# Kernel tuning notes

Measured on AMD Instinct MI355X. Metric: run time of the kernel, lower is better.

## Reference

```python
import jax, jax.numpy as jnp
import numpy as np

WIDTH = 384  # reconstruction grid is WIDTH x WIDTH


def _conv2d(x, w, b, pad):
    y = jax.lax.conv_general_dilated(
        x, w, window_strides=(1, 1), padding=[(pad, pad), (pad, pad)],
        dimension_numbers=('NCHW', 'OIHW', 'NCHW'))
    return y + b[None, :, None, None]


def _backproject(sino, angles, width):
    """Pixel-driven flat-detector fan-beam backprojection with linear interp.
    torch-radon FanBeam defaults: src_dist = det_dist = det_count,
    det_spacing = (src_dist + det_dist) / src_dist.
    sino: [B, C, A, D] -> image [B, C, width, width]."""
    B, C, A, D = sino.shape
    dsrc = float(D)
    ddet = float(D)
    spacing = (dsrc + ddet) / dsrc  # = 2.0
    c = jnp.arange(width, dtype=sino.dtype) - (width - 1) / 2.0
    X = c[None, None, :]   # [1,1,W] image x
    Y = c[None, :, None]   # [1,W,1] image y
    cb = jnp.cos(angles)[:, None, None]  # [A,1,1]
    sb = jnp.sin(angles)[:, None, None]
    px = cb * X + sb * Y    # pixel coords in rotated (source) frame, [A,W,W]
    py = -sb * X + cb * Y
    # fractional detector coordinate of the ray source->pixel
    s = px * ((dsrc + ddet) / spacing) / (dsrc + py) + (D - 1) / 2.0
    i0 = jnp.floor(s)
    frac = s - i0
    i0 = i0.astype(jnp.int32)
    i1 = i0 + 1
    WW = width * width
    w0 = jnp.where((i0 >= 0) & (i0 < D), 1.0 - frac, 0.0).reshape(A, WW)
    w1 = jnp.where((i1 >= 0) & (i1 < D), frac, 0.0).reshape(A, WW)
    i0c = jnp.clip(i0, 0, D - 1).reshape(A, WW)
    i1c = jnp.clip(i1, 0, D - 1).reshape(A, WW)

    def gather(idx):
        return jnp.take_along_axis(
            sino, jnp.broadcast_to(idx[None, None], (B, C, A, WW)), axis=3)

    out = (gather(i0c) * w0 + gather(i1c) * w1).sum(axis=2)  # sum over angles
    return out.reshape(B, C, width, width)


def setup_inputs() -> dict:
    key = jax.random.key(0)
    ks = jax.random.split(key, 5)
    A, D = 192, 576
    sino = jax.random.normal(ks[0], (1, 1, A, D), dtype=jnp.float32)
    angles = (jnp.arange(A, dtype=jnp.float32) * (2.0 * np.pi / A))
    w1 = jax.random.normal(ks[1], (16, 1, 5, 5), dtype=jnp.float32) * 0.05
    b1 = jnp.zeros((16,), dtype=jnp.float32)
    w2 = jax.random.normal(ks[2], (1, 16, 5, 5), dtype=jnp.float32) * 0.05
    b2 = jnp.zeros((1,), dtype=jnp.float32)
    w3 = jax.random.normal(ks[3], (1, 2, 3, 3), dtype=jnp.float32) * 0.05
    b3 = jnp.zeros((1,), dtype=jnp.float32)
    return {"sino": sino, "angles": angles, "w1": w1, "b1": b1,
            "w2": w2, "b2": b2, "w3": w3, "b3": b3}


def reference(sino, angles, w1, b1, w2, b2, w3, b3):
    img = _backproject(sino, angles, WIDTH)
    h = _conv2d(sino, w1, b1, pad=2)
    sino_pred = _conv2d(h, w2, b2, pad=2)
    img_sino = _backproject(sino_pred, angles, WIDTH)
    img_pred = _conv2d(jnp.concatenate([img, img_sino], axis=1), w3, b3, pad=1)
    return (sino_pred, img_sino, img_pred)
```

## Files before the change

### kernel.cpp

```cpp
#include <hip/hip_runtime.h>

#define A_N 192
#define D_N 576
#define W_N 384
#define NPIX (W_N * W_N)
#define NSIN (A_N * D_N)
#define RSTR 580

__global__ __launch_bounds__(256, 1) void conv9_kernel(
    const float* __restrict__ sino, const float* __restrict__ angles,
    const float* __restrict__ w1, const float* __restrict__ b1,
    const float* __restrict__ w2, const float* __restrict__ b2,
    float* __restrict__ sino_pred, float2* __restrict__ inter,
    float4* __restrict__ tab)
{
    __shared__ float t[16][40];
    __shared__ float sw1[400], sw2[400], sb1[16];
    __shared__ float K[625], wsb1[25];
    __shared__ float Wcs[9][81];
    __shared__ float biasc[9];

    int tid = threadIdx.x;
    int byi = blockIdx.x / 18;
    int bxi = blockIdx.x % 18;
    int y0 = byi * 8, x0 = bxi * 32;

    if (blockIdx.x == 0) {
        if (tid < A_N) {
            float s, c;
            sincosf(angles[tid], &s, &c);
            tab[tid] = make_float4(c, s, fmaf(576.f, c, -287.5f * s),
                                         fmaf(576.f, s,  287.5f * c));
        }
        for (int i = tid; i < A_N * 4; i += 256) {
            int a = i >> 2, j = i & 3;
            inter[a * RSTR + (j < 2 ? j : 576 + j)] = make_float2(0.f, 0.f);
        }
    }

    for (int i = tid; i < 640; i += 256) {
        int r = i / 40, c = i - r * 40;
        int gy = y0 - 4 + r, gx = x0 - 4 + c;
        t[r][c] = (gy >= 0 && gy < A_N && gx >= 0 && gx < D_N)
                ? sino[gy * D_N + gx] : 0.f;
    }
    for (int i = tid; i < 400; i += 256) { sw1[i] = w1[i]; sw2[i] = w2[i]; }
    if (tid < 16) sb1[tid] = b1[tid];
    __syncthreads();

    for (int i = tid; i < 625; i += 256) {
        int q = i / 25, r = i - q * 25;
        float acc = 0.f;
        #pragma unroll
        for (int c = 0; c < 16; ++c)
            acc = fmaf(sw2[c * 25 + q], sw1[c * 25 + r], acc);
        K[i] = acc;
    }
    if (tid < 25) {
        float acc = 0.f;
        #pragma unroll
        for (int c = 0; c < 16; ++c) acc = fmaf(sw2[c * 25 + tid], sb1[c], acc);
        wsb1[tid] = acc;
    }
    __syncthreads();

    int ylo = (y0 == 0) ? 0 : 2, yhi = (y0 == A_N - 8) ? 4 : 2;
    int xlo = (x0 == 0) ? 0 : 2, xhi = (x0 == D_N - 32) ? 4 : 2;
    int nx = xhi - xlo + 1;
    int nc = (yhi - ylo + 1) * nx;

    for (int e = tid; e < nc * 81; e += 256) {
        int ci = e / 81, s = e - ci * 81;
        int yc = ylo + ci / nx, xc = xlo + ci % nx;
        int sy = s / 9 - 4, sx = s % 9 - 4;
        float acc = 0.f;
        for (int qy = -2; qy <= 2; ++qy) {
            if ((yc == 0 && qy < 0) || (yc == 1 && qy < -1) ||
                (yc == 3 && qy > 1) || (yc == 4 && qy > 0)) continue;
            int vy = sy - qy; if (vy < -2 || vy > 2) continue;
            for (int qx = -2; qx <= 2; ++qx) {
                if ((xc == 0 && qx < 0) || (xc == 1 && qx < -1) ||
                    (xc == 3 && qx > 1) || (xc == 4 && qx > 0)) continue;
                int vx = sx - qx; if (vx < -2 || vx > 2) continue;
                acc += K[((qy + 2) * 5 + qx + 2) * 25 + (vy + 2) * 5 + (vx + 2)];
            }
        }
        Wcs[ci][s] = acc;
    }
    if (tid < nc) {
        int yc = ylo + tid / nx, xc = xlo + tid % nx;
        float acc = b2[0];
        for (int qy = -2; qy <= 2; ++qy) {
            if ((yc == 0 && qy < 0) || (yc == 1 && qy < -1) ||
                (yc == 3 && qy > 1) || (yc == 4 && qy > 0)) continue;
            for (int qx = -2; qx <= 2; ++qx) {
                if ((xc == 0 && qx < 0) || (xc == 1 && qx < -1) ||
                    (xc == 3 && qx > 1) || (xc == 4 && qx > 0)) continue;
                acc += wsb1[(qy + 2) * 5 + qx + 2];
            }
        }
        biasc[tid] = acc;
    }
    __syncthreads();

    int lr = tid >> 5, lc = tid & 31;
    int gy = y0 + lr, gx = x0 + lc;
    int yc = (gy <= 1) ? gy : ((gy >= A_N - 2) ? (gy - (A_N - 5)) : 2);
    int xc = (gx <= 1) ? gx : ((gx >= D_N - 2) ? (gx - (D_N - 5)) : 2);
    int ci = (yc - ylo) * nx + (xc - xlo);
    float acc = biasc[ci];
    const float* Wp = Wcs[ci];
    #pragma unroll
    for (int sy = 0; sy < 9; ++sy)
        #pragma unroll
        for (int sx = 0; sx < 9; ++sx)
            acc = fmaf(t[lr + sy][lc + sx], Wp[sy * 9 + sx], acc);
    sino_pred[gy * D_N + gx] = acc;
    inter[gy * RSTR + 2 + gx] = make_float2(t[lr + 4][lc + 4], acc);
}

__global__ __launch_bounds__(256) void backproject2_kernel(
    const float2* __restrict__ inter, const float4* __restrict__ tab,
    float2* __restrict__ part2)
{
    int tid = threadIdx.x;
    int seg = blockIdx.z;
    int a0 = seg * 64;
    int tx = tid & 15, ty = tid >> 4;
    int gx = blockIdx.x * 16 + tx;
    int gy = blockIdx.y * 16 + ty;
    int idx = gy * W_N + gx;
    float X = (float)gx - 191.5f;
    float Y = (float)gy - 191.5f;
    float acc0 = 0.f, acc1 = 0.f;
    const float2* base = inter + (size_t)a0 * RSTR + 2;
    #pragma unroll 8
    for (int i = 0; i < 64; ++i) {
        float4 tb = tab[a0 + i];
        float den = fmaf(tb.x, Y, fmaf(-tb.y, X, 576.f));
        float num = fmaf(tb.z, X, fmaf(tb.w, Y, 165600.f));
        float s   = num * __builtin_amdgcn_rcpf(den);
        float sc  = fminf(fmaxf(s, -2.f), 576.f);
        float fl  = floorf(sc);
        float fr  = sc - fl;
        int   ic  = (int)fl;
        float4 v = *reinterpret_cast<const float4*>(base + (size_t)i * RSTR + ic);
        acc0 = fmaf(v.x, 1.f - fr, fmaf(v.z, fr, acc0));
        acc1 = fmaf(v.y, 1.f - fr, fmaf(v.w, fr, acc1));
    }
    part2[seg * NPIX + idx] = make_float2(acc0, acc1);
}

__global__ __launch_bounds__(256) void conv3_kernel(
    const float2* __restrict__ part2,
    const float* __restrict__ w3, const float* __restrict__ b3,
    float* __restrict__ img_sino, float* __restrict__ img_pred)
{
    __shared__ float t0[10][34], t1[10][34];
    __shared__ float sw[18];
    int tid = threadIdx.x;
    int byi = blockIdx.x / 12, bxi = blockIdx.x % 12;
    int y0 = byi * 8, x0 = bxi * 32;
    for (int i = tid; i < 340; i += 256) {
        int r = i / 34, c = i - r * 34;
        int gy = y0 - 1 + r, gx = x0 - 1 + c;
        float s0 = 0.f, s1 = 0.f;
        if (gy >= 0 && gy < W_N && gx >= 0 && gx < W_N) {
            int g = gy * W_N + gx;
            #pragma unroll
            for (int p = 0; p < 3; ++p) {
                float2 v = part2[p * NPIX + g];
                s0 += v.x; s1 += v.y;
            }
        }
        t0[r][c] = s0; t1[r][c] = s1;
    }
    if (tid < 18) sw[tid] = w3[tid];
    __syncthreads();
    int lr = tid >> 5, lc = tid & 31;
    int gy = y0 + lr, gx = x0 + lc;
    int g = gy * W_N + gx;
    img_sino[g] = t1[lr + 1][lc + 1];
    float acc = b3[0];
    #pragma unroll
    for (int dy = 0; dy < 3; ++dy)
        #pragma unroll
        for (int dx = 0; dx < 3; ++dx) {
            acc = fmaf(t0[lr + dy][lc + dx], sw[dy * 3 + dx], acc);
            acc = fmaf(t1[lr + dy][lc + dx], sw[9 + dy * 3 + dx], acc);
        }
    img_pred[g] = acc;
}

extern "C" void kernel_launch(void* const* d_in, const int* in_sizes, int n_in,
                              void* d_out, int out_size, void* d_ws, size_t ws_size,
                              hipStream_t stream) {
    const float* sino   = (const float*)d_in[0];
    const float* angles = (const float*)d_in[1];
    const float* w1     = (const float*)d_in[2];
    const float* b1     = (const float*)d_in[3];
    const float* w2     = (const float*)d_in[4];
    const float* b2     = (const float*)d_in[5];
    const float* w3     = (const float*)d_in[6];
    const float* b3     = (const float*)d_in[7];

    float* out       = (float*)d_out;
    float* sino_pred = out;
    float* img_sino  = out + NSIN;
    float* img_pred  = img_sino + NPIX;

    float2* inter = (float2*)d_ws;
    float4* tab   = (float4*)((char*)d_ws + (size_t)A_N * RSTR * sizeof(float2));
    float2* part2 = (float2*)((char*)tab + A_N * sizeof(float4));

    conv9_kernel<<<dim3(432), dim3(256), 0, stream>>>(
        sino, angles, w1, b1, w2, b2, sino_pred, inter, tab);
    backproject2_kernel<<<dim3(24, 24, 3), dim3(256), 0, stream>>>(
        inter, tab, part2);
    conv3_kernel<<<dim3(576), dim3(256), 0, stream>>>(
        part2, w3, b3, img_sino, img_pred);
}
```

Measured before the change: 34.18 us.

## Fuse backprojection with 3x3 conv, recomputing halo pixels per tile

Merges the angle-split backprojection and the final 3x3 convolution into one kernel. Each 384-thread block backprojects an 18x18 tile (16x16 plus halo) over all angles into shared memory, then applies the conv. This removes a kernel launch and the global partial-sum buffer round trip. In exchange, halo pixels are backprojected redundantly (about 27% extra work) and angle-level parallelism is dropped.

```diff
diff --git a/kernel.cpp b/kernel.cpp
--- a/kernel.cpp
+++ b/kernel.cpp
@@ -119,77 +119,59 @@
     inter[gy * RSTR + 2 + gx] = make_float2(t[lr + 4][lc + 4], acc);
 }
 
-__global__ __launch_bounds__(256) void backproject2_kernel(
+__global__ __launch_bounds__(384) void bpc3_kernel(
     const float2* __restrict__ inter, const float4* __restrict__ tab,
-    float2* __restrict__ part2)
-{
-    int tid = threadIdx.x;
-    int seg = blockIdx.z;
-    int a0 = seg * 64;
-    int tx = tid & 15, ty = tid >> 4;
-    int gx = blockIdx.x * 16 + tx;
-    int gy = blockIdx.y * 16 + ty;
-    int idx = gy * W_N + gx;
-    float X = (float)gx - 191.5f;
-    float Y = (float)gy - 191.5f;
-    float acc0 = 0.f, acc1 = 0.f;
-    const float2* base = inter + (size_t)a0 * RSTR + 2;
-    #pragma unroll 8
-    for (int i = 0; i < 64; ++i) {
-        float4 tb = tab[a0 + i];
-        float den = fmaf(tb.x, Y, fmaf(-tb.y, X, 576.f));
-        float num = fmaf(tb.z, X, fmaf(tb.w, Y, 165600.f));
-        float s   = num * __builtin_amdgcn_rcpf(den);
-        float sc  = fminf(fmaxf(s, -2.f), 576.f);
-        float fl  = floorf(sc);
-        float fr  = sc - fl;
-        int   ic  = (int)fl;
-        float4 v = *reinterpret_cast<const float4*>(base + (size_t)i * RSTR + ic);
-        acc0 = fmaf(v.x, 1.f - fr, fmaf(v.z, fr, acc0));
-        acc1 = fmaf(v.y, 1.f - fr, fmaf(v.w, fr, acc1));
-    }
-    part2[seg * NPIX + idx] = make_float2(acc0, acc1);
-}
-
-__global__ __launch_bounds__(256) void conv3_kernel(
-    const float2* __restrict__ part2,
     const float* __restrict__ w3, const float* __restrict__ b3,
     float* __restrict__ img_sino, float* __restrict__ img_pred)
 {
-    __shared__ float t0[10][34], t1[10][34];
+    __shared__ float t0s[18][19], t1s[18][19];
     __shared__ float sw[18];
     int tid = threadIdx.x;
-    int byi = blockIdx.x / 12, bxi = blockIdx.x % 12;
-    int y0 = byi * 8, x0 = bxi * 32;
-    for (int i = tid; i < 340; i += 256) {
-        int r = i / 34, c = i - r * 34;
-        int gy = y0 - 1 + r, gx = x0 - 1 + c;
-        float s0 = 0.f, s1 = 0.f;
-        if (gy >= 0 && gy < W_N && gx >= 0 && gx < W_N) {
-            int g = gy * W_N + gx;
+    if (tid < 18) sw[tid] = w3[tid];
+    if (tid < 324) {
+        int r = tid / 18, c = tid - r * 18;
+        int gy = blockIdx.y * 16 - 1 + r;
+        int gx = blockIdx.x * 16 - 1 + c;
+        float X = (float)gx - 191.5f;
+        float Y = (float)gy - 191.5f;
+        float acc0 = 0.f, acc1 = 0.f;
+        const float2* base = inter + 2;
+        #pragma unroll 8
+        for (int a = 0; a < A_N; ++a) {
+            float4 tb = tab[a];
+            float den = fmaf(tb.x, Y, fmaf(-tb.y, X, 576.f));
+            float num = fmaf(tb.z, X, fmaf(tb.w, Y, 165600.f));
+            float s   = num * __builtin_amdgcn_rcpf(den);
+            float sc  = fminf(fmaxf(s, -2.f), 576.f);
+            float fl  = floorf(sc);
+            float fr  = sc - fl;
+            int   ic  = (int)fl;
+            float4 v = *reinterpret_cast<const float4*>(base + (size_t)a * RSTR + ic);
+            float w0 = 1.f - fr;
+            acc0 = fmaf(v.x, w0, fmaf(v.z, fr, acc0));
+            acc1 = fmaf(v.y, w0, fmaf(v.w, fr, acc1));
+        }
+        bool inside = (gy >= 0 && gy < W_N && gx >= 0 && gx < W_N);
+        t0s[r][c] = inside ? acc0 : 0.f;
+        t1s[r][c] = inside ? acc1 : 0.f;
+    }
+    __syncthreads();
+    if (tid < 256) {
+        int lr = tid >> 4, lc = tid & 15;
+        int gy = blockIdx.y * 16 + lr;
+        int gx = blockIdx.x * 16 + lc;
+        int g = gy * W_N + gx;
+        img_sino[g] = t1s[lr + 1][lc + 1];
+        float acc = b3[0];
+        #pragma unroll
+        for (int dy = 0; dy < 3; ++dy)
             #pragma unroll
-            for (int p = 0; p < 3; ++p) {
-                float2 v = part2[p * NPIX + g];
-                s0 += v.x; s1 += v.y;
+            for (int dx = 0; dx < 3; ++dx) {
+                acc = fmaf(t0s[lr + dy][lc + dx], sw[dy * 3 + dx], acc);
+                acc = fmaf(t1s[lr + dy][lc + dx], sw[9 + dy * 3 + dx], acc);
             }
-        }
-        t0[r][c] = s0; t1[r][c] = s1;
-    }
-    if (tid < 18) sw[tid] = w3[tid];
-    __syncthreads();
-    int lr = tid >> 5, lc = tid & 31;
-    int gy = y0 + lr, gx = x0 + lc;
-    int g = gy * W_N + gx;
-    img_sino[g] = t1[lr + 1][lc + 1];
-    float acc = b3[0];
-    #pragma unroll
-    for (int dy = 0; dy < 3; ++dy)
-        #pragma unroll
-        for (int dx = 0; dx < 3; ++dx) {
-            acc = fmaf(t0[lr + dy][lc + dx], sw[dy * 3 + dx], acc);
-            acc = fmaf(t1[lr + dy][lc + dx], sw[9 + dy * 3 + dx], acc);
-        }
-    img_pred[g] = acc;
+        img_pred[g] = acc;
+    }
 }
 
 extern "C" void kernel_launch(void* const* d_in, const int* in_sizes, int n_in,
@@ -211,12 +193,9 @@
 
     float2* inter = (float2*)d_ws;
     float4* tab   = (float4*)((char*)d_ws + (size_t)A_N * RSTR * sizeof(float2));
-    float2* part2 = (float2*)((char*)tab + A_N * sizeof(float4));
 
     conv9_kernel<<<dim3(432), dim3(256), 0, stream>>>(
         sino, angles, w1, b1, w2, b2, sino_pred, inter, tab);
-    backproject2_kernel<<<dim3(24, 24, 3), dim3(256), 0, stream>>>(
-        inter, tab, part2);
-    conv3_kernel<<<dim3(576), dim3(256), 0, stream>>>(
-        part2, w3, b3, img_sino, img_pred);
+    bpc3_kernel<<<dim3(24, 24), dim3(384), 0, stream>>>(
+        inter, tab, w3, b3, img_sino, img_pred);
 }
```

New measurement: 44.82 us. 31.1% more time.
